# Kernel optimization log

Hardware: AMD Instinct MI355X
Metric: run time of the kernel (lower is better)

## Reference

```python
import jax, jax.numpy as jnp
import numpy as np

D_MODEL = 1024
N_HEADS = 16
CHUNK = 64
EPS = 1e-6


def elu_plus_1(x):
    return jax.nn.elu(x) + 1.0


def setup_inputs() -> dict:
    key = jax.random.key(0)
    kx, kq, kk, kv, ko = jax.random.split(key, 5)
    B, T = 4, 4096
    # xavier_uniform for square (D, D) weights: limit = sqrt(6/(D+D))
    lim = float(np.sqrt(6.0 / (D_MODEL + D_MODEL)))
    mk = lambda k: jax.random.uniform(k, (D_MODEL, D_MODEL), jnp.float32, -lim, lim)
    return {
        "x": jax.random.normal(kx, (B, T, D_MODEL), jnp.float32),
        "W_q": mk(kq),
        "W_k": mk(kk),
        "W_v": mk(kv),
        "W_o": mk(ko),
    }


def reference(x, W_q, W_k, W_v, W_o):
    B, T, D = x.shape
    H = N_HEADS
    dk = D // H
    dv = dk
    C = CHUNK
    N = T // C  # T chosen divisible by chunk size (no padding needed)

    q = (x @ W_q.T).reshape(B, T, H, dk)
    k = (x @ W_k.T).reshape(B, T, H, dk)
    v = (x @ W_v.T).reshape(B, T, H, dv)

    phi_q = elu_plus_1(q).reshape(B, N, C, H, dk)
    phi_k = elu_plus_1(k).reshape(B, N, C, H, dk)
    vc = v.reshape(B, N, C, H, dv)

    # Per-chunk key-value outer products and key sums, then exclusive prefix
    # sums over chunks give the carried state S and normalizer z at each
    # chunk's start (same math as the sequential chunk loop).
    KV = jnp.einsum('bnchk,bnchv->bnhkv', phi_k, vc)      # (B,N,H,dk,dv)
    Ksum = phi_k.sum(axis=2)                               # (B,N,C->sum,H,dk) -> (B,N,H,dk)
    KV_cum = jnp.cumsum(KV, axis=1)
    Ksum_cum = jnp.cumsum(Ksum, axis=1)
    S_prefix = jnp.concatenate([jnp.zeros_like(KV_cum[:, :1]), KV_cum[:, :-1]], axis=1)
    z_prefix = jnp.concatenate([jnp.zeros_like(Ksum_cum[:, :1]), Ksum_cum[:, :-1]], axis=1)

    # Inter-chunk contribution from carried state
    inter = jnp.einsum('bnchk,bnhkv->bnchv', phi_q, S_prefix)   # (B,N,C,H,dv)
    z_inter = jnp.einsum('bnchk,bnhk->bnch', phi_q, z_prefix)   # (B,N,C,H)

    # Intra-chunk causal attention
    mask = jnp.tril(jnp.ones((C, C), dtype=x.dtype))
    attn = jnp.einsum('bnihk,bnjhk->bnhij', phi_q, phi_k) * mask  # (B,N,H,C,C)
    intra = jnp.einsum('bnhij,bnjhv->bnihv', attn, vc)            # (B,N,C,H,dv)
    z_intra = attn.sum(axis=-1).transpose(0, 1, 3, 2)             # (B,N,C,H)

    denom = jnp.clip((z_inter + z_intra)[..., None], 1e-6, None)
    y = (inter + intra) / denom                                   # (B,N,C,H,dv)
    y = y.reshape(B, T, H * dv)
    return y @ W_o.T
```

## Files before the change

kernel.cpp:

```cpp
#include <hip/hip_runtime.h>


typedef unsigned short u16;
typedef float  f32x4 __attribute__((ext_vector_type(4)));
typedef short  b16x8 __attribute__((ext_vector_type(8)));
typedef u16    u16x4 __attribute__((ext_vector_type(4)));
typedef u16    u16x8 __attribute__((ext_vector_type(8)));

#define DEVINL __device__ __forceinline__

DEVINL u16 f2b(float f) {
  unsigned u = __float_as_uint(f);
  return (u16)((u + 0x7fffu + ((u >> 16) & 1u)) >> 16);
}
DEVINL float b2f(u16 s) { return __uint_as_float(((unsigned)s) << 16); }

DEVINL f32x4 mfma16(b16x8 a, b16x8 b, f32x4 c) {
  return __builtin_amdgcn_mfma_f32_16x16x32_bf16(a, b, c, 0, 0, 0);
}

DEVINL float phi_elu1(float v) { return v > 0.f ? v + 1.f : __expf(v); }

__global__ void cvt_kernel(const float* __restrict__ in, u16* __restrict__ out, int n8) {
  int stride = gridDim.x * blockDim.x;
  for (int i = blockIdx.x * blockDim.x + threadIdx.x; i < n8; i += stride) {
    const float* p = in + (size_t)i * 8;
    f32x4 a = *(const f32x4*)p;
    f32x4 b = *(const f32x4*)(p + 4);
    u16x8 o;
    o[0] = f2b(a[0]); o[1] = f2b(a[1]); o[2] = f2b(a[2]); o[3] = f2b(a[3]);
    o[4] = f2b(b[0]); o[5] = f2b(b[1]); o[6] = f2b(b[2]); o[7] = f2b(b[3]);
    *(u16x8*)(out + (size_t)i * 8) = o;
  }
}

template <bool PHI, typename OT>
__global__ __launch_bounds__(512, 2) void gemm256(const u16* __restrict__ A,
                                                  const u16* __restrict__ B,
                                                  OT* __restrict__ C, int M, int N) {
  __shared__ char lds[131072];
  const int tid = threadIdx.x, wid = tid >> 6, l = tid & 63;
  const int l15 = l & 15, lg = l >> 4;
  const int wr = wid >> 2, wc = wid & 3;
  const int ntn = N >> 8;
  const int nwg = gridDim.x, bid = blockIdx.x;
  const int cpx = nwg >> 3;
  const int sb = (bid & 7) * cpx + (bid >> 3);
  const int tm = sb / ntn, tn = sb - tm * ntn;

  const int colX0 = (lg * 16) ^ ((l15 & 7) << 4);
  const int colX1 = (64 + lg * 16) ^ ((l15 & 7) << 4);
  char* ldsA = lds + wr * 16384 + l15 * 128;
  char* ldsB = lds + 32768 + (wc >> 1) * 16384 + ((wc & 1) * 64 + l15) * 128;

  const int srow = tid >> 3;
  const int scol = ((((tid & 7) * 16) ^ ((srow & 7) << 4)) >> 1);
  const u16* sA = A + (size_t)(tm * 256 + srow) * 1024 + scol;
  const u16* sB = B + (size_t)(tn * 256 + srow) * 1024 + scol;
  char* ldsStage = lds + wid * 1024;

#define STAGE(tt, h)                                                            \
  do {                                                                          \
    const u16* s_ = ((h) < 2 ? sA : sB) + (size_t)(((h) & 1) * 128) * 1024 +    \
                    (size_t)(tt) * 64;                                          \
    char* d_ = ldsStage + (((tt) & 1) << 16) + ((h) < 2 ? 0 : 32768) +          \
               (((h) & 1) << 14);                                               \
    __builtin_amdgcn_global_load_lds(                                           \
        (const __attribute__((address_space(1))) void*)(s_),                    \
        (__attribute__((address_space(3))) void*)(d_), 16, 0, 0);               \
    __builtin_amdgcn_global_load_lds(                                           \
        (const __attribute__((address_space(1))) void*)(s_ + 64 * 1024),        \
        (__attribute__((address_space(3))) void*)(d_ + 8192), 16, 0, 0);        \
  } while (0)

  f32x4 acc[8][4];
#pragma unroll
  for (int i = 0; i < 8; i++)
#pragma unroll
    for (int j = 0; j < 4; j++) acc[i][j] = f32x4{0.f, 0.f, 0.f, 0.f};

  STAGE(0, 0); STAGE(0, 1); STAGE(0, 2); STAGE(0, 3);
  STAGE(1, 2); STAGE(1, 3);
  asm volatile("s_waitcnt vmcnt(4)" ::: "memory");
  __builtin_amdgcn_s_barrier();

  b16x8 a0[4], a1[4], b0[4], b1[4];
  for (int t = 0; t < 16; ++t) {
    const int cb = (t & 1) << 16;
#pragma unroll
    for (int fm = 0; fm < 4; fm++) a0[fm] = *(const b16x8*)(ldsA + cb + fm * 2048 + colX0);
#pragma unroll
    for (int fn = 0; fn < 4; fn++) b0[fn] = *(const b16x8*)(ldsB + cb + fn * 2048 + colX0);
    if (t < 15) STAGE(t + 1, 0);
    __builtin_amdgcn_s_barrier();
    asm volatile("s_waitcnt lgkmcnt(0)" ::: "memory");
    __builtin_amdgcn_sched_barrier(0);
    __builtin_amdgcn_s_setprio(1);
#pragma unroll
    for (int fm = 0; fm < 4; fm++)
#pragma unroll
      for (int fn = 0; fn < 4; fn++) acc[fm][fn] = mfma16(a0[fm], b0[fn], acc[fm][fn]);
    __builtin_amdgcn_s_setprio(0);
    __builtin_amdgcn_s_barrier();
#pragma unroll
    for (int fm = 0; fm < 4; fm++) a1[fm] = *(const b16x8*)(ldsA + cb + (4 + fm) * 2048 + colX0);
#pragma unroll
    for (int fn = 0; fn < 4; fn++) b1[fn] = *(const b16x8*)(ldsB + cb + fn * 2048 + colX1);
    if (t < 15) STAGE(t + 1, 1);
    __builtin_amdgcn_s_barrier();
    asm volatile("s_waitcnt lgkmcnt(0)" ::: "memory");
    __builtin_amdgcn_sched_barrier(0);
    __builtin_amdgcn_s_setprio(1);
#pragma unroll
    for (int fm = 0; fm < 4; fm++)
#pragma unroll
      for (int fn = 0; fn < 4; fn++) acc[4 + fm][fn] = mfma16(a1[fm], b0[fn], acc[4 + fm][fn]);
    __builtin_amdgcn_s_setprio(0);
    __builtin_amdgcn_s_barrier();
#pragma unroll
    for (int fm = 0; fm < 4; fm++) a0[fm] = *(const b16x8*)(ldsA + cb + fm * 2048 + colX1);
    if (t < 14) STAGE(t + 2, 2);
    __builtin_amdgcn_s_barrier();
    asm volatile("s_waitcnt lgkmcnt(0)" ::: "memory");
    __builtin_amdgcn_sched_barrier(0);
    __builtin_amdgcn_s_setprio(1);
#pragma unroll
    for (int fm = 0; fm < 4; fm++)
#pragma unroll
      for (int fn = 0; fn < 4; fn++) acc[fm][fn] = mfma16(a0[fm], b1[fn], acc[fm][fn]);
    __builtin_amdgcn_s_setprio(0);
    __builtin_amdgcn_s_barrier();
#pragma unroll
    for (int fm = 0; fm < 4; fm++) a1[fm] = *(const b16x8*)(ldsA + cb + (4 + fm) * 2048 + colX1);
    if (t < 14) STAGE(t + 2, 3);
    __builtin_amdgcn_s_barrier();
    asm volatile("s_waitcnt lgkmcnt(0)" ::: "memory");
    __builtin_amdgcn_sched_barrier(0);
    __builtin_amdgcn_s_setprio(1);
#pragma unroll
    for (int fm = 0; fm < 4; fm++)
#pragma unroll
      for (int fn = 0; fn < 4; fn++) acc[4 + fm][fn] = mfma16(a1[fm], b1[fn], acc[4 + fm][fn]);
    __builtin_amdgcn_s_setprio(0);
    if (t < 14) asm volatile("s_waitcnt vmcnt(4)" ::: "memory");
    else        asm volatile("s_waitcnt vmcnt(0)" ::: "memory");
    __builtin_amdgcn_s_barrier();
  }
#undef STAGE

#pragma unroll
  for (int fm = 0; fm < 8; ++fm)
#pragma unroll
    for (int fn = 0; fn < 4; ++fn)
#pragma unroll
      for (int r = 0; r < 4; ++r) {
        size_t grow = (size_t)tm * 256 + wr * 128 + fm * 16 + lg * 4 + r;
        size_t gcol = (size_t)tn * 256 + wc * 64 + fn * 16 + l15;
        float v = acc[fm][fn][r];
        if (PHI) v = phi_elu1(v);
        OT* p = C + grow * (size_t)N + gcol;
        if constexpr (sizeof(OT) == 2) *p = (OT)f2b(v);
        else                           *p = (OT)v;
      }
}

__global__ __launch_bounds__(256) void transpose64(const u16* __restrict__ in,
                                                   u16* __restrict__ out) {
  __shared__ u16 tile[64][68];
  const int t = threadIdx.x;
  const int tr = blockIdx.x, tc = blockIdx.y;
#pragma unroll
  for (int i = 0; i < 4; i++) {
    int idx = i * 256 + t, r = idx >> 4, c4 = idx & 15;
    u16x4 v = *(const u16x4*)(in + (size_t)(tr * 64 + r) * 1024 + tc * 64 + c4 * 4);
    *(u16x4*)&tile[r][c4 * 4] = v;
  }
  __syncthreads();
#pragma unroll
  for (int i = 0; i < 4; i++) {
    int idx = i * 256 + t, oc = idx >> 4, r4 = idx & 15;
    u16x4 v;
    v[0] = tile[r4 * 4 + 0][oc]; v[1] = tile[r4 * 4 + 1][oc];
    v[2] = tile[r4 * 4 + 2][oc]; v[3] = tile[r4 * 4 + 3][oc];
    *(u16x4*)(out + (size_t)(tc * 64 + oc) * 16384 + tr * 64 + r4 * 4) = v;
  }
}

__global__ __launch_bounds__(256, 2) void kv_kernel(const u16* __restrict__ kT,
                                                    const u16* __restrict__ vT,
                                                    u16* __restrict__ KVT,
                                                    float* __restrict__ Ksum) {
  const int tid = threadIdx.x, wid = tid >> 6, l = tid & 63, l15 = l & 15, lg = l >> 4;
  const int bid = blockIdx.x, hg = bid & 3, bn = bid >> 2, n = bn & 63, b = bn >> 6;
  const int h = hg * 4 + wid;
  const size_t cb = (size_t)b * 4096 + n * 64 + lg * 8;

  b16x8 af[4][2], bf[4][2];
#pragma unroll
  for (int fm = 0; fm < 4; fm++)
#pragma unroll
    for (int ks = 0; ks < 2; ks++)
      af[fm][ks] = *(const b16x8*)(vT + (size_t)(h * 64 + fm * 16 + l15) * 16384 + cb + ks * 32);
#pragma unroll
  for (int fn = 0; fn < 4; fn++)
#pragma unroll
    for (int ks = 0; ks < 2; ks++)
      bf[fn][ks] = *(const b16x8*)(kT + (size_t)(h * 64 + fn * 16 + l15) * 16384 + cb + ks * 32);

  f32x4 acc[4][4];
#pragma unroll
  for (int i = 0; i < 4; i++)
#pragma unroll
    for (int j = 0; j < 4; j++) acc[i][j] = f32x4{0.f, 0.f, 0.f, 0.f};
#pragma unroll
  for (int ks = 0; ks < 2; ks++)
#pragma unroll
    for (int fm = 0; fm < 4; fm++)
#pragma unroll
      for (int fn = 0; fn < 4; fn++) acc[fm][fn] = mfma16(af[fm][ks], bf[fn][ks], acc[fm][fn]);

  float ksum[4] = {0.f, 0.f, 0.f, 0.f};
#pragma unroll
  for (int fn = 0; fn < 4; fn++) {
#pragma unroll
    for (int ks = 0; ks < 2; ks++)
#pragma unroll
      for (int j = 0; j < 8; j++) ksum[fn] += b2f((u16)bf[fn][ks][j]);
    ksum[fn] += __shfl_xor(ksum[fn], 16);
    ksum[fn] += __shfl_xor(ksum[fn], 32);
  }
  const size_t ob = (size_t)(b * 64 + n) * 16 + h;
  if (l < 16) {
#pragma unroll
    for (int fn = 0; fn < 4; fn++) Ksum[ob * 64 + fn * 16 + l15] = ksum[fn];
  }
#pragma unroll
  for (int fm = 0; fm < 4; fm++)
#pragma unroll
    for (int fn = 0; fn < 4; fn++)
#pragma unroll
      for (int r = 0; r < 4; r++)
        KVT[ob * 4096 + (size_t)(fm * 16 + lg * 4 + r) * 64 + fn * 16 + l15] =
            f2b(acc[fm][fn][r]);
}

__global__ __launch_bounds__(256) void scan_s(const u16* __restrict__ KVT,
                                              u16* __restrict__ ST) {
  const int bh = blockIdx.x >> 4, slice = blockIdx.x & 15;
  const int b = bh >> 4, h = bh & 15;
  const int e = slice * 256 + threadIdx.x;
  float acc = 0.f;
  for (int n = 0; n < 64; n++) {
    size_t idx = ((size_t)(b * 64 + n) * 16 + h) * 4096 + e;
    ST[idx] = f2b(acc);
    acc += b2f(KVT[idx]);
  }
}

__global__ __launch_bounds__(64) void scan_z(const float* __restrict__ Ksum,
                                             float* __restrict__ zpre) {
  const int b = blockIdx.x >> 4, h = blockIdx.x & 15;
  const int t = threadIdx.x;
  float acc = 0.f;
  for (int n = 0; n < 64; n++) {
    size_t idx = ((size_t)(b * 64 + n) * 16 + h) * 64 + t;
    zpre[idx] = acc;
    acc += Ksum[idx];
  }
}

__global__ __launch_bounds__(256, 2) void attn_out(const u16* __restrict__ phiQ,
                                                   const u16* __restrict__ phiK,
                                                   const u16* __restrict__ vT,
                                                   const u16* __restrict__ ST,
                                                   const float* __restrict__ zpre,
                                                   u16* __restrict__ Y) {
  __shared__ char lds[4 * 8192 + 4 * 256];
  const int tid = threadIdx.x, wid = tid >> 6, l = tid & 63, l15 = l & 15, lg = l >> 4;
  const int bid = blockIdx.x, hg = bid & 3, bn = bid >> 2, n = bn & 63, b = bn >> 6;
  const int h = hg * 4 + wid;
  const size_t row0 = (size_t)b * 4096 + n * 64;
  const int dcol = h * 64;

  b16x8 qf[4][2];
#pragma unroll
  for (int fi = 0; fi < 4; fi++)
#pragma unroll
    for (int ks = 0; ks < 2; ks++)
      qf[fi][ks] = *(const b16x8*)(phiQ + (row0 + fi * 16 + l15) * 1024 + dcol + lg * 8 + ks * 32);

  f32x4 accT[4][4];
#pragma unroll
  for (int i = 0; i < 4; i++)
#pragma unroll
    for (int j = 0; j < 4; j++) accT[i][j] = f32x4{0.f, 0.f, 0.f, 0.f};
  {
    b16x8 kf[4][2];
#pragma unroll
    for (int fj = 0; fj < 4; fj++)
#pragma unroll
      for (int ks = 0; ks < 2; ks++)
        kf[fj][ks] = *(const b16x8*)(phiK + (row0 + fj * 16 + l15) * 1024 + dcol + lg * 8 + ks * 32);
#pragma unroll
    for (int ks = 0; ks < 2; ks++)
#pragma unroll
      for (int fj = 0; fj < 4; fj++)
#pragma unroll
        for (int fi = 0; fi < 4; fi++)
          accT[fj][fi] = mfma16(kf[fj][ks], qf[fi][ks], accT[fj][fi]);
  }

  const size_t zb = ((size_t)(b * 64 + n) * 16 + h) * 64;
  float zi[4] = {0.f, 0.f, 0.f, 0.f};
#pragma unroll
  for (int ks = 0; ks < 2; ks++) {
    f32x4 z0 = *(const f32x4*)(zpre + zb + lg * 8 + ks * 32);
    f32x4 z1 = *(const f32x4*)(zpre + zb + lg * 8 + ks * 32 + 4);
#pragma unroll
    for (int fi = 0; fi < 4; fi++)
#pragma unroll
      for (int j = 0; j < 4; j++) {
        zi[fi] += b2f((u16)qf[fi][ks][j])     * z0[j];
        zi[fi] += b2f((u16)qf[fi][ks][j + 4]) * z1[j];
      }
  }

  char* abuf = lds + wid * 8192;
  float zt[4] = {0.f, 0.f, 0.f, 0.f};
#pragma unroll
  for (int fi = 0; fi < 4; fi++) {
    const int i = fi * 16 + l15;
    const int swz = (i & 7) << 4;
#pragma unroll
    for (int fj = 0; fj < 4; fj++) {
      f32x4 v = accT[fj][fi];
#pragma unroll
      for (int r = 0; r < 4; r++) {
        int j = fj * 16 + lg * 4 + r;
        if (j > i) v[r] = 0.f;
        zt[fi] += v[r];
      }
      unsigned w0 = (unsigned)f2b(v[0]) | ((unsigned)f2b(v[1]) << 16);
      unsigned w1 = (unsigned)f2b(v[2]) | ((unsigned)f2b(v[3]) << 16);
      int jb = (fj * 16 + lg * 4) * 2;
      *(unsigned*)(abuf + i * 128 + (jb ^ swz)) = w0;
      *(unsigned*)(abuf + i * 128 + ((jb + 4) ^ swz)) = w1;
    }
  }

  float* dbuf = (float*)(lds + 32768 + wid * 256);
#pragma unroll
  for (int fi = 0; fi < 4; fi++) {
    float z = zi[fi] + zt[fi];
    z += __shfl_xor(z, 16);
    z += __shfl_xor(z, 32);
    float rd = 1.f / fmaxf(z, 1e-6f);
    if (l < 16) dbuf[fi * 16 + l15] = rd;
  }
  __syncthreads();

  b16x8 stf[4][2], vf[4][2];
  const size_t stb = ((size_t)(b * 64 + n) * 16 + h) * 4096;
#pragma unroll
  for (int fn = 0; fn < 4; fn++)
#pragma unroll
    for (int ks = 0; ks < 2; ks++) {
      stf[fn][ks] = *(const b16x8*)(ST + stb + (size_t)(fn * 16 + l15) * 64 + lg * 8 + ks * 32);
      vf[fn][ks]  = *(const b16x8*)(vT + (size_t)(dcol + fn * 16 + l15) * 16384 +
                                    (size_t)b * 4096 + n * 64 + lg * 8 + ks * 32);
    }
  f32x4 acc[4][4];
#pragma unroll
  for (int i = 0; i < 4; i++)
#pragma unroll
    for (int j = 0; j < 4; j++) acc[i][j] = f32x4{0.f, 0.f, 0.f, 0.f};
#pragma unroll
  for (int ks = 0; ks < 2; ks++)
#pragma unroll
    for (int fm = 0; fm < 4; fm++)
#pragma unroll
      for (int fn = 0; fn < 4; fn++) acc[fm][fn] = mfma16(qf[fm][ks], stf[fn][ks], acc[fm][fn]);
#pragma unroll
  for (int fm = 0; fm < 4; fm++) {
    const int i = fm * 16 + l15;
    const int swz = (i & 7) << 4;
#pragma unroll
    for (int ks = 0; ks < 2; ks++) {
      b16x8 af = *(const b16x8*)(abuf + i * 128 + ((ks * 64 + lg * 16) ^ swz));
#pragma unroll
      for (int fn = 0; fn < 4; fn++) acc[fm][fn] = mfma16(af, vf[fn][ks], acc[fm][fn]);
    }
  }

#pragma unroll
  for (int fm = 0; fm < 4; fm++)
#pragma unroll
    for (int r = 0; r < 4; r++) {
      float rd = dbuf[fm * 16 + lg * 4 + r];
#pragma unroll
      for (int fn = 0; fn < 4; fn++)
        Y[(row0 + fm * 16 + lg * 4 + r) * 1024 + dcol + fn * 16 + l15] =
            f2b(acc[fm][fn][r] * rd);
    }
}

extern "C" void kernel_launch(void* const* d_in, const int* in_sizes, int n_in,
                              void* d_out, int out_size, void* d_ws, size_t ws_size,
                              hipStream_t stream) {
  const float* x  = (const float*)d_in[0];
  const float* Wq = (const float*)d_in[1];
  const float* Wk = (const float*)d_in[2];
  const float* Wv = (const float*)d_in[3];
  const float* Wo = (const float*)d_in[4];
  float* out = (float*)d_out;

  char* ws = (char*)d_ws;
  size_t off = 0;
  auto alloc = [&](size_t bytes) -> char* {
    char* p = ws + off;
    off += (bytes + 255) & ~(size_t)255;
    return p;
  };
  u16*   xb   = (u16*)alloc(33554432);
  u16*   wqb  = (u16*)alloc(2097152);
  u16*   wkb  = (u16*)alloc(2097152);
  u16*   wvb  = (u16*)alloc(2097152);
  u16*   wob  = (u16*)alloc(2097152);
  u16*   phiQ = (u16*)alloc(33554432);
  u16*   phiK = (u16*)alloc(33554432);
  u16*   vT   = (u16*)alloc(33554432);
  u16*   kT   = (u16*)alloc(33554432);
  u16*   KVT  = (u16*)alloc(33554432);
  float* Ksum = (float*)alloc(1048576);
  u16*   ST   = (u16*)alloc(33554432);
  float* zpre = (float*)alloc(1048576);
  u16*   y    = xb;

  cvt_kernel<<<2048, 256, 0, stream>>>(x, xb, 2097152);
  cvt_kernel<<<512, 256, 0, stream>>>(Wq, wqb, 131072);
  cvt_kernel<<<512, 256, 0, stream>>>(Wk, wkb, 131072);
  cvt_kernel<<<512, 256, 0, stream>>>(Wv, wvb, 131072);
  cvt_kernel<<<512, 256, 0, stream>>>(Wo, wob, 131072);

  gemm256<true, u16><<<256, 512, 0, stream>>>(xb, wqb, phiQ, 16384, 1024);
  gemm256<true, u16><<<256, 512, 0, stream>>>(xb, wkb, phiK, 16384, 1024);
  gemm256<false, u16><<<256, 512, 0, stream>>>(wvb, xb, vT, 1024, 16384);

  transpose64<<<dim3(256, 16), 256, 0, stream>>>(phiK, kT);
  kv_kernel<<<1024, 256, 0, stream>>>(kT, vT, KVT, Ksum);
  scan_s<<<1024, 256, 0, stream>>>(KVT, ST);
  scan_z<<<64, 64, 0, stream>>>(Ksum, zpre);
  attn_out<<<1024, 256, 0, stream>>>(phiQ, phiK, vT, ST, zpre, y);

  gemm256<false, float><<<256, 512, 0, stream>>>(y, wob, out, 16384, 1024);
}
```

Measured before the change: 252.3 us.

## Add 128x128 GEMM, merge weight casts, reorder KV state layout per head

Adds a new 128x128-tile GEMM that loads global memory directly into LDS and uses it for the Q projection and the output projection, replacing the 256x256 kernel in those two calls. The four weight conversion launches are merged into one kernel that selects its tensor from the y grid index. The KV and Ksum buffers are laid out as (b,h,n) instead of (b,n,h), so each scan reads contiguous chunks, and scan_s prefetches four chunks ahead. Together these aim to cut launch overhead, raise GEMM occupancy or tile count, and improve scan memory locality. The risk is that the new GEMM has no double buffering, so it may be slower than the tuned 256 tile.

```diff
diff --git a/kernel.cpp b/kernel.cpp
--- a/kernel.cpp
+++ b/kernel.cpp
@@ -32,6 +32,106 @@
     o[4] = f2b(b[0]); o[5] = f2b(b[1]); o[6] = f2b(b[2]); o[7] = f2b(b[3]);
     *(u16x8*)(out + (size_t)i * 8) = o;
   }
+}
+
+__global__ void cvt4_kernel(const float* __restrict__ p0, const float* __restrict__ p1,
+                            const float* __restrict__ p2, const float* __restrict__ p3,
+                            u16* __restrict__ o0, u16* __restrict__ o1,
+                            u16* __restrict__ o2, u16* __restrict__ o3) {
+  const float* in; u16* out;
+  switch (blockIdx.y) {
+    case 0: in = p0; out = o0; break;
+    case 1: in = p1; out = o1; break;
+    case 2: in = p2; out = o2; break;
+    default: in = p3; out = o3; break;
+  }
+  int i = blockIdx.x * blockDim.x + threadIdx.x;
+  const float* p = in + (size_t)i * 8;
+  f32x4 a = *(const f32x4*)p;
+  f32x4 b = *(const f32x4*)(p + 4);
+  u16x8 o;
+  o[0] = f2b(a[0]); o[1] = f2b(a[1]); o[2] = f2b(a[2]); o[3] = f2b(a[3]);
+  o[4] = f2b(b[0]); o[5] = f2b(b[1]); o[6] = f2b(b[2]); o[7] = f2b(b[3]);
+  *(u16x8*)(out + (size_t)i * 8) = o;
+}
+
+template <bool PHI, typename OT>
+__global__ __launch_bounds__(256, 2) void gemm_bt(const u16* __restrict__ A,
+                                                  const u16* __restrict__ B,
+                                                  OT* __restrict__ C, int M, int N) {
+  __shared__ char lds[32768];
+  const int tid = threadIdx.x, wid = tid >> 6, l = tid & 63;
+  const int l15 = l & 15, lg = l >> 4;
+  const int ntn = N >> 7;
+  const int nwg = gridDim.x, bid = blockIdx.x;
+  const int cpx = nwg >> 3;
+  const int sb = (bid & 7) * cpx + (bid >> 3);
+  const int tm = sb / ntn, tn = sb - tm * ntn;
+  const int wr = wid >> 1, wc = wid & 1;
+
+  f32x4 acc[4][4];
+#pragma unroll
+  for (int i = 0; i < 4; i++)
+#pragma unroll
+    for (int j = 0; j < 4; j++) acc[i][j] = f32x4{0.f, 0.f, 0.f, 0.f};
+
+  const u16* sptr[8];
+#pragma unroll
+  for (int i = 0; i < 8; i++) {
+    int sidx = wid * 8 + i;
+    int o = sidx * 1024 + l * 16;
+    int lo = o & 16383;
+    int row = lo >> 7;
+    int cb = (lo & 127) ^ ((row & 7) << 4);
+    sptr[i] = (o < 16384 ? A + (size_t)(tm * 128 + row) * 1024
+                         : B + (size_t)(tn * 128 + row) * 1024) + (cb >> 1);
+  }
+
+  for (int kt = 0; kt < 16; ++kt) {
+    const int k0 = kt * 64;
+#pragma unroll
+    for (int i = 0; i < 8; i++) {
+      __builtin_amdgcn_global_load_lds(
+          (const __attribute__((address_space(1))) void*)(sptr[i] + k0),
+          (__attribute__((address_space(3))) void*)(lds + (wid * 8 + i) * 1024),
+          16, 0, 0);
+    }
+    __syncthreads();
+#pragma unroll
+    for (int ks = 0; ks < 2; ++ks) {
+      b16x8 af[4], bf[4];
+#pragma unroll
+      for (int fm = 0; fm < 4; ++fm) {
+        int row = wr * 64 + fm * 16 + l15;
+        af[fm] = *(const b16x8*)(lds + row * 128 + ((ks * 64 + lg * 16) ^ ((row & 7) << 4)));
+      }
+#pragma unroll
+      for (int fn = 0; fn < 4; ++fn) {
+        int row = wc * 64 + fn * 16 + l15;
+        bf[fn] = *(const b16x8*)(lds + 16384 + row * 128 + ((ks * 64 + lg * 16) ^ ((row & 7) << 4)));
+      }
+#pragma unroll
+      for (int fm = 0; fm < 4; ++fm)
+#pragma unroll
+        for (int fn = 0; fn < 4; ++fn) acc[fm][fn] = mfma16(af[fm], bf[fn], acc[fm][fn]);
+    }
+    __syncthreads();
+  }
+
+#pragma unroll
+  for (int fm = 0; fm < 4; ++fm)
+#pragma unroll
+    for (int fn = 0; fn < 4; ++fn)
+#pragma unroll
+      for (int r = 0; r < 4; ++r) {
+        size_t grow = tm * 128 + wr * 64 + fm * 16 + lg * 4 + r;
+        size_t gcol = tn * 128 + wc * 64 + fn * 16 + l15;
+        float v = acc[fm][fn][r];
+        if (PHI) v = phi_elu1(v);
+        OT* p = C + grow * (size_t)N + gcol;
+        if constexpr (sizeof(OT) == 2) *p = (OT)f2b(v);
+        else                           *p = (OT)v;
+      }
 }
 
 template <bool PHI, typename OT>
@@ -229,7 +329,7 @@
     ksum[fn] += __shfl_xor(ksum[fn], 16);
     ksum[fn] += __shfl_xor(ksum[fn], 32);
   }
-  const size_t ob = (size_t)(b * 64 + n) * 16 + h;
+  const size_t ob = (size_t)(b * 16 + h) * 64 + n;
   if (l < 16) {
 #pragma unroll
     for (int fn = 0; fn < 4; fn++) Ksum[ob * 64 + fn * 16 + l15] = ksum[fn];
@@ -246,24 +346,37 @@
 
 __global__ __launch_bounds__(256) void scan_s(const u16* __restrict__ KVT,
                                               u16* __restrict__ ST) {
-  const int bh = blockIdx.x >> 4, slice = blockIdx.x & 15;
-  const int b = bh >> 4, h = bh & 15;
-  const int e = slice * 256 + threadIdx.x;
+  const size_t base = (size_t)(blockIdx.x >> 4) * 64 * 4096 +
+                      (blockIdx.x & 15) * 256 + threadIdx.x;
   float acc = 0.f;
-  for (int n = 0; n < 64; n++) {
-    size_t idx = ((size_t)(b * 64 + n) * 16 + h) * 4096 + e;
-    ST[idx] = f2b(acc);
-    acc += b2f(KVT[idx]);
+  float v[4], w[4];
+#pragma unroll
+  for (int i = 0; i < 4; i++) v[i] = b2f(KVT[base + (size_t)i * 4096]);
+  for (int n = 0; n < 64; n += 4) {
+    if (n < 60) {
+#pragma unroll
+      for (int i = 0; i < 4; i++) w[i] = b2f(KVT[base + (size_t)(n + 4 + i) * 4096]);
+    } else {
+#pragma unroll
+      for (int i = 0; i < 4; i++) w[i] = 0.f;
+    }
+#pragma unroll
+    for (int i = 0; i < 4; i++) {
+      ST[base + (size_t)(n + i) * 4096] = f2b(acc);
+      acc += v[i];
+    }
+#pragma unroll
+    for (int i = 0; i < 4; i++) v[i] = w[i];
   }
 }
 
 __global__ __launch_bounds__(64) void scan_z(const float* __restrict__ Ksum,
                                              float* __restrict__ zpre) {
-  const int b = blockIdx.x >> 4, h = blockIdx.x & 15;
+  const size_t bh = blockIdx.x;
   const int t = threadIdx.x;
   float acc = 0.f;
   for (int n = 0; n < 64; n++) {
-    size_t idx = ((size_t)(b * 64 + n) * 16 + h) * 64 + t;
+    size_t idx = (bh * 64 + n) * 64 + t;
     zpre[idx] = acc;
     acc += Ksum[idx];
   }
@@ -310,7 +423,7 @@
           accT[fj][fi] = mfma16(kf[fj][ks], qf[fi][ks], accT[fj][fi]);
   }
 
-  const size_t zb = ((size_t)(b * 64 + n) * 16 + h) * 64;
+  const size_t zb = ((size_t)(b * 16 + h) * 64 + n) * 64;
   float zi[4] = {0.f, 0.f, 0.f, 0.f};
 #pragma unroll
   for (int ks = 0; ks < 2; ks++) {
@@ -360,7 +473,7 @@
   __syncthreads();
 
   b16x8 stf[4][2], vf[4][2];
-  const size_t stb = ((size_t)(b * 64 + n) * 16 + h) * 4096;
+  const size_t stb = ((size_t)(b * 16 + h) * 64 + n) * 4096;
 #pragma unroll
   for (int fn = 0; fn < 4; fn++)
 #pragma unroll
@@ -437,20 +550,15 @@
   u16*   y    = xb;
 
   cvt_kernel<<<2048, 256, 0, stream>>>(x, xb, 2097152);
-  cvt_kernel<<<512, 256, 0, stream>>>(Wq, wqb, 131072);
-  cvt_kernel<<<512, 256, 0, stream>>>(Wk, wkb, 131072);
-  cvt_kernel<<<512, 256, 0, stream>>>(Wv, wvb, 131072);
-  cvt_kernel<<<512, 256, 0, stream>>>(Wo, wob, 131072);
-
-  gemm256<true, u16><<<256, 512, 0, stream>>>(xb, wqb, phiQ, 16384, 1024);
+  cvt4_kernel<<<dim3(512, 4), 256, 0, stream>>>(Wq, Wk, Wv, Wo, wqb, wkb, wvb, wob);
+
+  gemm_bt<true, u16><<<1024, 256, 0, stream>>>(xb, wqb, phiQ, 16384, 1024);
   gemm256<true, u16><<<256, 512, 0, stream>>>(xb, wkb, phiK, 16384, 1024);
   gemm256<false, u16><<<256, 512, 0, stream>>>(wvb, xb, vT, 1024, 16384);
-
   transpose64<<<dim3(256, 16), 256, 0, stream>>>(phiK, kT);
   kv_kernel<<<1024, 256, 0, stream>>>(kT, vT, KVT, Ksum);
   scan_s<<<1024, 256, 0, stream>>>(KVT, ST);
   scan_z<<<64, 64, 0, stream>>>(Ksum, zpre);
   attn_out<<<1024, 256, 0, stream>>>(phiQ, phiK, vT, ST, zpre, y);
-
-  gemm256<false, float><<<256, 512, 0, stream>>>(y, wob, out, 16384, 1024);
-}
+  gemm_bt<false, float><<<1024, 256, 0, stream>>>(y, wob, out, 16384, 1024);
+}
```

Result: no change. 252.1 us (-0.1%).

## Merge weight conversions, relayout KV/state to (b,h,n), prefetch scan, drop GEMM lgkm waits

Applied to the files above, without the earlier changes.

Folds the four weight-conversion launches into one 2D-grid kernel to cut launch overhead. Changes the KVT/ST/Ksum/zpre layout to batch-head-major with the chunk index next, so the scans stride contiguously, and adds a four-deep register prefetch in scan_s. In the GEMM main loop it removes the explicit lgkmcnt(0) waits after barriers and adds sched_barriers instead. Dropping those waits relies on the compiler inserting the waits needed before LDS reads are consumed, which could change correctness or scheduling.

```diff
diff --git a/kernel.cpp b/kernel.cpp
--- a/kernel.cpp
+++ b/kernel.cpp
@@ -32,6 +32,27 @@
     o[4] = f2b(b[0]); o[5] = f2b(b[1]); o[6] = f2b(b[2]); o[7] = f2b(b[3]);
     *(u16x8*)(out + (size_t)i * 8) = o;
   }
+}
+
+__global__ void cvt4_kernel(const float* __restrict__ p0, const float* __restrict__ p1,
+                            const float* __restrict__ p2, const float* __restrict__ p3,
+                            u16* __restrict__ o0, u16* __restrict__ o1,
+                            u16* __restrict__ o2, u16* __restrict__ o3) {
+  const float* in; u16* out;
+  switch (blockIdx.y) {
+    case 0: in = p0; out = o0; break;
+    case 1: in = p1; out = o1; break;
+    case 2: in = p2; out = o2; break;
+    default: in = p3; out = o3; break;
+  }
+  int i = blockIdx.x * blockDim.x + threadIdx.x;
+  const float* p = in + (size_t)i * 8;
+  f32x4 a = *(const f32x4*)p;
+  f32x4 b = *(const f32x4*)(p + 4);
+  u16x8 o;
+  o[0] = f2b(a[0]); o[1] = f2b(a[1]); o[2] = f2b(a[2]); o[3] = f2b(a[3]);
+  o[4] = f2b(b[0]); o[5] = f2b(b[1]); o[6] = f2b(b[2]); o[7] = f2b(b[3]);
+  *(u16x8*)(out + (size_t)i * 8) = o;
 }
 
 template <bool PHI, typename OT>
@@ -73,6 +94,12 @@
         (__attribute__((address_space(3))) void*)(d_ + 8192), 16, 0, 0);        \
   } while (0)
 
+#define BAR_SB()                                                                \
+  do {                                                                          \
+    __builtin_amdgcn_s_barrier();                                               \
+    __builtin_amdgcn_sched_barrier(0);                                          \
+  } while (0)
+
   f32x4 acc[8][4];
 #pragma unroll
   for (int i = 0; i < 8; i++)
@@ -82,7 +109,7 @@
   STAGE(0, 0); STAGE(0, 1); STAGE(0, 2); STAGE(0, 3);
   STAGE(1, 2); STAGE(1, 3);
   asm volatile("s_waitcnt vmcnt(4)" ::: "memory");
-  __builtin_amdgcn_s_barrier();
+  BAR_SB();
 
   b16x8 a0[4], a1[4], b0[4], b1[4];
   for (int t = 0; t < 16; ++t) {
@@ -92,50 +119,42 @@
 #pragma unroll
     for (int fn = 0; fn < 4; fn++) b0[fn] = *(const b16x8*)(ldsB + cb + fn * 2048 + colX0);
     if (t < 15) STAGE(t + 1, 0);
-    __builtin_amdgcn_s_barrier();
-    asm volatile("s_waitcnt lgkmcnt(0)" ::: "memory");
-    __builtin_amdgcn_sched_barrier(0);
+    BAR_SB();
     __builtin_amdgcn_s_setprio(1);
 #pragma unroll
     for (int fm = 0; fm < 4; fm++)
 #pragma unroll
       for (int fn = 0; fn < 4; fn++) acc[fm][fn] = mfma16(a0[fm], b0[fn], acc[fm][fn]);
     __builtin_amdgcn_s_setprio(0);
-    __builtin_amdgcn_s_barrier();
+    BAR_SB();
 #pragma unroll
     for (int fm = 0; fm < 4; fm++) a1[fm] = *(const b16x8*)(ldsA + cb + (4 + fm) * 2048 + colX0);
 #pragma unroll
     for (int fn = 0; fn < 4; fn++) b1[fn] = *(const b16x8*)(ldsB + cb + fn * 2048 + colX1);
     if (t < 15) STAGE(t + 1, 1);
-    __builtin_amdgcn_s_barrier();
-    asm volatile("s_waitcnt lgkmcnt(0)" ::: "memory");
-    __builtin_amdgcn_sched_barrier(0);
+    BAR_SB();
     __builtin_amdgcn_s_setprio(1);
 #pragma unroll
     for (int fm = 0; fm < 4; fm++)
 #pragma unroll
       for (int fn = 0; fn < 4; fn++) acc[4 + fm][fn] = mfma16(a1[fm], b0[fn], acc[4 + fm][fn]);
     __builtin_amdgcn_s_setprio(0);
-    __builtin_amdgcn_s_barrier();
+    BAR_SB();
 #pragma unroll
     for (int fm = 0; fm < 4; fm++) a0[fm] = *(const b16x8*)(ldsA + cb + fm * 2048 + colX1);
     if (t < 14) STAGE(t + 2, 2);
-    __builtin_amdgcn_s_barrier();
-    asm volatile("s_waitcnt lgkmcnt(0)" ::: "memory");
-    __builtin_amdgcn_sched_barrier(0);
+    BAR_SB();
     __builtin_amdgcn_s_setprio(1);
 #pragma unroll
     for (int fm = 0; fm < 4; fm++)
 #pragma unroll
       for (int fn = 0; fn < 4; fn++) acc[fm][fn] = mfma16(a0[fm], b1[fn], acc[fm][fn]);
     __builtin_amdgcn_s_setprio(0);
-    __builtin_amdgcn_s_barrier();
+    BAR_SB();
 #pragma unroll
     for (int fm = 0; fm < 4; fm++) a1[fm] = *(const b16x8*)(ldsA + cb + (4 + fm) * 2048 + colX1);
     if (t < 14) STAGE(t + 2, 3);
-    __builtin_amdgcn_s_barrier();
-    asm volatile("s_waitcnt lgkmcnt(0)" ::: "memory");
-    __builtin_amdgcn_sched_barrier(0);
+    BAR_SB();
     __builtin_amdgcn_s_setprio(1);
 #pragma unroll
     for (int fm = 0; fm < 4; fm++)
@@ -144,9 +163,10 @@
     __builtin_amdgcn_s_setprio(0);
     if (t < 14) asm volatile("s_waitcnt vmcnt(4)" ::: "memory");
     else        asm volatile("s_waitcnt vmcnt(0)" ::: "memory");
-    __builtin_amdgcn_s_barrier();
+    BAR_SB();
   }
 #undef STAGE
+#undef BAR_SB
 
 #pragma unroll
   for (int fm = 0; fm < 8; ++fm)
@@ -229,7 +249,7 @@
     ksum[fn] += __shfl_xor(ksum[fn], 16);
     ksum[fn] += __shfl_xor(ksum[fn], 32);
   }
-  const size_t ob = (size_t)(b * 64 + n) * 16 + h;
+  const size_t ob = (size_t)(b * 16 + h) * 64 + n;
   if (l < 16) {
 #pragma unroll
     for (int fn = 0; fn < 4; fn++) Ksum[ob * 64 + fn * 16 + l15] = ksum[fn];
@@ -246,24 +266,37 @@
 
 __global__ __launch_bounds__(256) void scan_s(const u16* __restrict__ KVT,
                                               u16* __restrict__ ST) {
-  const int bh = blockIdx.x >> 4, slice = blockIdx.x & 15;
-  const int b = bh >> 4, h = bh & 15;
-  const int e = slice * 256 + threadIdx.x;
+  const size_t base = (size_t)(blockIdx.x >> 4) * 64 * 4096 +
+                      (blockIdx.x & 15) * 256 + threadIdx.x;
   float acc = 0.f;
-  for (int n = 0; n < 64; n++) {
-    size_t idx = ((size_t)(b * 64 + n) * 16 + h) * 4096 + e;
-    ST[idx] = f2b(acc);
-    acc += b2f(KVT[idx]);
+  float v[4], w[4];
+#pragma unroll
+  for (int i = 0; i < 4; i++) v[i] = b2f(KVT[base + (size_t)i * 4096]);
+  for (int n = 0; n < 64; n += 4) {
+    if (n < 60) {
+#pragma unroll
+      for (int i = 0; i < 4; i++) w[i] = b2f(KVT[base + (size_t)(n + 4 + i) * 4096]);
+    } else {
+#pragma unroll
+      for (int i = 0; i < 4; i++) w[i] = 0.f;
+    }
+#pragma unroll
+    for (int i = 0; i < 4; i++) {
+      ST[base + (size_t)(n + i) * 4096] = f2b(acc);
+      acc += v[i];
+    }
+#pragma unroll
+    for (int i = 0; i < 4; i++) v[i] = w[i];
   }
 }
 
 __global__ __launch_bounds__(64) void scan_z(const float* __restrict__ Ksum,
                                              float* __restrict__ zpre) {
-  const int b = blockIdx.x >> 4, h = blockIdx.x & 15;
+  const size_t bh = blockIdx.x;
   const int t = threadIdx.x;
   float acc = 0.f;
   for (int n = 0; n < 64; n++) {
-    size_t idx = ((size_t)(b * 64 + n) * 16 + h) * 64 + t;
+    size_t idx = (bh * 64 + n) * 64 + t;
     zpre[idx] = acc;
     acc += Ksum[idx];
   }
@@ -310,7 +343,7 @@
           accT[fj][fi] = mfma16(kf[fj][ks], qf[fi][ks], accT[fj][fi]);
   }
 
-  const size_t zb = ((size_t)(b * 64 + n) * 16 + h) * 64;
+  const size_t zb = ((size_t)(b * 16 + h) * 64 + n) * 64;
   float zi[4] = {0.f, 0.f, 0.f, 0.f};
 #pragma unroll
   for (int ks = 0; ks < 2; ks++) {
@@ -360,7 +393,7 @@
   __syncthreads();
 
   b16x8 stf[4][2], vf[4][2];
-  const size_t stb = ((size_t)(b * 64 + n) * 16 + h) * 4096;
+  const size_t stb = ((size_t)(b * 16 + h) * 64 + n) * 4096;
 #pragma unroll
   for (int fn = 0; fn < 4; fn++)
 #pragma unroll
@@ -437,10 +470,7 @@
   u16*   y    = xb;
 
   cvt_kernel<<<2048, 256, 0, stream>>>(x, xb, 2097152);
-  cvt_kernel<<<512, 256, 0, stream>>>(Wq, wqb, 131072);
-  cvt_kernel<<<512, 256, 0, stream>>>(Wk, wkb, 131072);
-  cvt_kernel<<<512, 256, 0, stream>>>(Wv, wvb, 131072);
-  cvt_kernel<<<512, 256, 0, stream>>>(Wo, wob, 131072);
+  cvt4_kernel<<<dim3(512, 4), 256, 0, stream>>>(Wq, Wk, Wv, Wo, wqb, wkb, wvb, wob);
 
   gemm256<true, u16><<<256, 512, 0, stream>>>(xb, wqb, phiQ, 16384, 1024);
   gemm256<true, u16><<<256, 512, 0, stream>>>(xb, wkb, phiK, 16384, 1024);
```

After: 247.6 us. Within noise of the previous version (-1.9%).
